# Performance work log

Measured on AMD Instinct MI355X. Metric: run time of the kernel, lower is better.

Reference implementation:

```python
import jax, jax.numpy as jnp
import numpy as np

IGNORE_INDEX = -100
BETA = 0.1

def setup_inputs() -> dict:
    key = jax.random.key(0)
    k1, k2, k3, k4, k5, k6 = jax.random.split(key, 6)
    B, T, H, V = 4, 512, 2048, 32000
    x = jax.random.normal(k1, (B, T, H), dtype=jnp.float32)
    ref_x = jax.random.normal(k2, (B, T, H), dtype=jnp.float32)
    y = jax.random.randint(k3, (B, T), 0, V, dtype=jnp.int64)
    # mask a prefix of each sequence with ignore_index to exercise masking
    y = y.at[:, :10].set(IGNORE_INDEX)
    preference_labels = jax.random.randint(k4, (B,), 0, 2) == 1
    scale = 1.0 / np.sqrt(H)
    W = jax.random.normal(k5, (V, H), dtype=jnp.float32) * scale      # policy lm_head weight
    ref_W = jax.random.normal(k6, (V, H), dtype=jnp.float32) * scale  # reference lm_head weight
    return {"x": x, "ref_x": ref_x, "y": y, "preference_labels": preference_labels,
            "W": W, "ref_W": ref_W}


def _avg_target_logps(inp, w, y):
    # inp: (B, T, H), w: (V, H), y: (B, T) -> per-sequence average log-prob (B,)
    logits = jnp.einsum("bth,vh->btv", inp, w)
    logps = jax.nn.log_softmax(logits.astype(jnp.float32), axis=-1)
    mask = y != IGNORE_INDEX
    labels = jnp.where(mask, y, 0)
    tok_logps = jnp.take_along_axis(logps, labels[..., None], axis=-1)[..., 0]
    return (tok_logps * mask).sum(-1) / mask.sum(-1)


def reference(x, ref_x, y, preference_labels, W, ref_W):
    policy_logps = _avg_target_logps(x, W, y)                              # (B,)
    ref_logps = jax.lax.stop_gradient(_avg_target_logps(ref_x, ref_W, y))  # ref model under no_grad
    logratios = policy_logps - ref_logps
    multiplier = jnp.where(preference_labels, 1.0, -1.0)
    # KTO loss with KL term = 0 (policy_KL_logps / ref_KL_logps are None)
    losses = 1.0 - jax.nn.sigmoid(BETA * logratios * multiplier)
    return losses.sum() / y.shape[0]
```

## Files before the change

### kernel.cpp

```cpp
#include <hip/hip_runtime.h>
#include <math.h>

#define BATCH 4
#define TSEQ 512
#define MTOK 2048
#define HDIM 2048
#define VOCAB 32000
#define NCHUNK 500
#define IGNORE_INDEX (-100)
#define BETA 0.1f

#define CVT_PER_BLOCK 8192
#define WCVT_BLK (VOCAB * HDIM / 4 / CVT_PER_BLOCK)
#define XCVT_BLK (MTOK * HDIM / 4 / CVT_PER_BLOCK)

typedef __attribute__((ext_vector_type(4))) float floatx4;
typedef __attribute__((ext_vector_type(8))) short short8;
typedef __attribute__((ext_vector_type(4))) unsigned short ushortx4;

__device__ __forceinline__ unsigned short f2bf(float f) {
    unsigned int u = __float_as_uint(f);
    u += 0x7fffu + ((u >> 16) & 1u);
    return (unsigned short)(u >> 16);
}

__device__ __forceinline__ void async_copy16(const unsigned short* g, unsigned short* l) {
    __builtin_amdgcn_global_load_lds(
        (const __attribute__((address_space(1))) void*)g,
        (__attribute__((address_space(3))) void*)l, 16, 0, 0);
}

__device__ __forceinline__ void cvt_run(const float* __restrict__ src,
                                        unsigned short* __restrict__ dst,
                                        int relblk) {
    size_t base = (size_t)relblk * CVT_PER_BLOCK + threadIdx.x;
    const floatx4* s4 = (const floatx4*)src;
    ushortx4* d4 = (ushortx4*)dst;
#pragma unroll
    for (int k = 0; k < 32; ++k) {
        floatx4 a = s4[base + k * 256];
        ushortx4 o;
        o[0] = f2bf(a[0]); o[1] = f2bf(a[1]);
        o[2] = f2bf(a[2]); o[3] = f2bf(a[3]);
        d4[base + k * 256] = o;
    }
}

__global__ __launch_bounds__(256) void cvt_all_kernel(
        const float* __restrict__ s0, const float* __restrict__ s1,
        const float* __restrict__ s2, const float* __restrict__ s3,
        unsigned short* __restrict__ d0, unsigned short* __restrict__ d1,
        unsigned short* __restrict__ d2, unsigned short* __restrict__ d3) {
    int b = blockIdx.x;
    if (b < WCVT_BLK)                   cvt_run(s0, d0, b);
    else if (b < 2 * WCVT_BLK)          cvt_run(s1, d1, b - WCVT_BLK);
    else if (b < 2 * WCVT_BLK + XCVT_BLK) cvt_run(s2, d2, b - 2 * WCVT_BLK);
    else                                cvt_run(s3, d3, b - 2 * WCVT_BLK - XCVT_BLK);
}

__global__ __launch_bounds__(256) void cvt_one_kernel(
        const float* __restrict__ src, unsigned short* __restrict__ dst) {
    cvt_run(src, dst, blockIdx.x);
}

#define BK 64
__global__ __launch_bounds__(256, 2) void gemm_lse_kernel(
        const unsigned short* __restrict__ Xb0,
        const unsigned short* __restrict__ Xb1,
        const unsigned short* __restrict__ Wb0,
        const unsigned short* __restrict__ Wb1,
        const int* __restrict__ y,
        float* __restrict__ pmax,
        float* __restrict__ psum,
        float* __restrict__ tlog,
        int slot_base)
{
    __shared__ __align__(16) unsigned short sA[128 * BK];
    __shared__ __align__(16) unsigned short sB[128 * BK];

    const int slot = slot_base + blockIdx.z;
    const unsigned short* __restrict__ Xb = slot ? Xb1 : Xb0;
    const unsigned short* __restrict__ Wb = slot ? Wb1 : Wb0;

    const int tid  = threadIdx.x;
    const int m0   = blockIdx.x * 128;
    const int v0   = blockIdx.y * 128;
    const int w    = tid >> 6;
    const int lane = tid & 63;
    const int wm   = w & 1;
    const int wn   = w >> 1;
    const int c    = lane & 15;
    const int q    = lane >> 4;

    floatx4 acc[4][4] = {};

    const int e0 = tid * 8;

    for (int kt = 0; kt < HDIM / BK; ++kt) {
        const int k0 = kt * BK;
#pragma unroll
        for (int it = 0; it < 4; ++it) {
            int e   = it * 2048 + e0;
            int row = e >> 6;
            int p   = (e >> 3) & 7;
            int col = (p ^ (row & 7)) * 8;
            async_copy16(Xb + (size_t)(m0 + row) * HDIM + (k0 + col), &sA[e]);
            async_copy16(Wb + (size_t)(v0 + row) * HDIM + (k0 + col), &sB[e]);
        }
        __syncthreads();
#pragma unroll
        for (int kk = 0; kk < BK; kk += 32) {
            short8 af[4], bf[4];
            const int gq = (kk >> 3) + q;
            const int pq = gq ^ (c & 7);
#pragma unroll
            for (int i = 0; i < 4; ++i)
                af[i] = *(const short8*)&sA[(wm * 64 + i * 16 + c) * BK + pq * 8];
#pragma unroll
            for (int j = 0; j < 4; ++j)
                bf[j] = *(const short8*)&sB[(wn * 64 + j * 16 + c) * BK + pq * 8];
#pragma unroll
            for (int i = 0; i < 4; ++i)
#pragma unroll
                for (int j = 0; j < 4; ++j)
                    acc[i][j] = __builtin_amdgcn_mfma_f32_16x16x32_bf16(
                        af[i], bf[j], acc[i][j], 0, 0, 0);
        }
        __syncthreads();
    }

    const int chunk = blockIdx.y * 2 + wn;
#pragma unroll
    for (int i = 0; i < 4; ++i) {
        float mx[4], sm[4];
#pragma unroll
        for (int r = 0; r < 4; ++r) {
            float m4 = acc[i][0][r];
            m4 = fmaxf(m4, acc[i][1][r]);
            m4 = fmaxf(m4, acc[i][2][r]);
            m4 = fmaxf(m4, acc[i][3][r]);
            mx[r] = m4;
        }
#pragma unroll
        for (int d = 1; d < 16; d <<= 1)
#pragma unroll
            for (int r = 0; r < 4; ++r)
                mx[r] = fmaxf(mx[r], __shfl_xor(mx[r], d, 64));
#pragma unroll
        for (int r = 0; r < 4; ++r) {
            float s = 0.f;
#pragma unroll
            for (int j = 0; j < 4; ++j) s += expf(acc[i][j][r] - mx[r]);
            sm[r] = s;
        }
#pragma unroll
        for (int d = 1; d < 16; d <<= 1)
#pragma unroll
            for (int r = 0; r < 4; ++r)
                sm[r] += __shfl_xor(sm[r], d, 64);

        const int tokenBase = m0 + wm * 64 + i * 16 + q * 4;
        if (c == 0) {
#pragma unroll
            for (int r = 0; r < 4; ++r) {
                pmax[(size_t)(slot * MTOK + tokenBase + r) * NCHUNK + chunk] = mx[r];
                psum[(size_t)(slot * MTOK + tokenBase + r) * NCHUNK + chunk] = sm[r];
            }
        }
#pragma unroll
        for (int r = 0; r < 4; ++r) {
            int lab = y[tokenBase + r];
            int rel = lab - (v0 + wn * 64);
            if (rel >= 0 && rel < 64 && (rel & 15) == c) {
#pragma unroll
                for (int j = 0; j < 4; ++j)
                    if ((rel >> 4) == j)
                        tlog[(size_t)slot * MTOK + tokenBase + r] = acc[i][j][r];
            }
        }
    }
}

__global__ __launch_bounds__(256) void finalize_kernel(
        const int* __restrict__ y,
        const float* __restrict__ pmax,
        const float* __restrict__ psum,
        const float* __restrict__ tlog,
        float* __restrict__ tokll, int slot_base) {
    const int wv    = threadIdx.x >> 6;
    const int lane  = threadIdx.x & 63;
    const int token = blockIdx.x * 4 + wv;
    const int slot  = slot_base + blockIdx.y;

    const float* pm = &pmax[(size_t)(slot * MTOK + token) * NCHUNK];
    const float* ps = &psum[(size_t)(slot * MTOK + token) * NCHUNK];
    float m = -3.4e38f, s = 0.f;
    for (int c2 = lane; c2 < NCHUNK; c2 += 64) {
        float cm = pm[c2];
        float cs = ps[c2];
        if (cm > m) { s = s * expf(m - cm) + cs; m = cm; }
        else        { s += cs * expf(cm - m); }
    }
#pragma unroll
    for (int d = 1; d < 64; d <<= 1) {
        float om = __shfl_xor(m, d, 64);
        float os = __shfl_xor(s, d, 64);
        if (om > m) { s = s * expf(m - om) + os; m = om; }
        else        { s += os * expf(om - m); }
    }
    if (lane == 0) {
        int lab = y[token];
        float lse = m + logf(s);
        tokll[(size_t)slot * MTOK + token] =
            (lab == IGNORE_INDEX) ? 0.f : (tlog[(size_t)slot * MTOK + token] - lse);
    }
}

__global__ __launch_bounds__(256) void tail_kernel(
        const int* __restrict__ y,
        const float* __restrict__ tokll,
        const int* __restrict__ pref,
        float* __restrict__ out) {
    __shared__ float rs[256];
    __shared__ float rc[256];
    __shared__ float seqavg[8];
    const int tid = threadIdx.x;
    for (int sb = 0; sb < 8; ++sb) {
        const int slot = sb >> 2;
        const int b    = sb & 3;
        float lsum = 0.f, lcnt = 0.f;
        for (int t = tid; t < TSEQ; t += 256) {
            int token = b * TSEQ + t;
            lsum += tokll[(size_t)slot * MTOK + token];
            lcnt += (y[token] != IGNORE_INDEX) ? 1.f : 0.f;
        }
        rs[tid] = lsum; rc[tid] = lcnt;
        __syncthreads();
        for (int s2 = 128; s2 > 0; s2 >>= 1) {
            if (tid < s2) { rs[tid] += rs[tid + s2]; rc[tid] += rc[tid + s2]; }
            __syncthreads();
        }
        if (tid == 0) seqavg[sb] = rs[0] / rc[0];
        __syncthreads();
    }
    if (tid == 0) {
        float acc = 0.f;
        for (int b = 0; b < BATCH; ++b) {
            float lr   = seqavg[b] - seqavg[BATCH + b];
            float mult = pref[b] ? 1.f : -1.f;
            float z    = BETA * lr * mult;
            float sig  = 1.f / (1.f + expf(-z));
            acc += 1.f - sig;
        }
        out[0] = acc * (1.f / (float)BATCH);
    }
}

extern "C" void kernel_launch(void* const* d_in, const int* in_sizes, int n_in,
                              void* d_out, int out_size, void* d_ws, size_t ws_size,
                              hipStream_t stream) {
    const float* x      = (const float*)d_in[0];
    const float* ref_x  = (const float*)d_in[1];
    const int*   y      = (const int*)d_in[2];
    const int*   pref   = (const int*)d_in[3];
    const float* W      = (const float*)d_in[4];
    const float* ref_W  = (const float*)d_in[5];
    float* out = (float*)d_out;
    char*  ws  = (char*)d_ws;

    const size_t WSZ = (size_t)VOCAB * HDIM * 2;
    const size_t XSZ = (size_t)MTOK * HDIM * 2;
    const size_t PSZ = (size_t)2 * MTOK * NCHUNK * 4;

    const size_t need_dual = 2*WSZ + 2*XSZ + 2*PSZ + (size_t)4*MTOK*4 + 4096;

    if (ws_size >= need_dual) {
        unsigned short* wbf0 = (unsigned short*)(ws);
        unsigned short* wbf1 = (unsigned short*)(ws + WSZ);
        unsigned short* xbf0 = (unsigned short*)(ws + 2*WSZ);
        unsigned short* xbf1 = (unsigned short*)(ws + 2*WSZ + XSZ);
        float* pmax  = (float*)(ws + 2*WSZ + 2*XSZ);
        float* psum  = (float*)(ws + 2*WSZ + 2*XSZ + PSZ);
        float* tlog  = (float*)(ws + 2*WSZ + 2*XSZ + 2*PSZ);
        float* tokll = (float*)(ws + 2*WSZ + 2*XSZ + 2*PSZ + (size_t)2*MTOK*4);

        cvt_all_kernel<<<2*WCVT_BLK + 2*XCVT_BLK, 256, 0, stream>>>(
            W, ref_W, x, ref_x, wbf0, wbf1, xbf0, xbf1);
        gemm_lse_kernel<<<dim3(MTOK/128, VOCAB/128, 2), 256, 0, stream>>>(
            xbf0, xbf1, wbf0, wbf1, y, pmax, psum, tlog, 0);
        finalize_kernel<<<dim3(MTOK/4, 2), 256, 0, stream>>>(
            y, pmax, psum, tlog, tokll, 0);
        tail_kernel<<<1, 256, 0, stream>>>(y, tokll, pref, out);
    } else {
        unsigned short* wbf = (unsigned short*)(ws);
        unsigned short* xbf = (unsigned short*)(ws + WSZ);
        float* pmax  = (float*)(ws + WSZ + XSZ);
        float* psum  = (float*)(ws + WSZ + XSZ + PSZ);
        float* tlog  = (float*)(ws + WSZ + XSZ + 2*PSZ);
        float* tokll = (float*)(ws + WSZ + XSZ + 2*PSZ + (size_t)2*MTOK*4);

        for (int model = 0; model < 2; ++model) {
            const float* xin = model ? ref_x : x;
            const float* win = model ? ref_W : W;
            cvt_one_kernel<<<WCVT_BLK, 256, 0, stream>>>(win, wbf);
            cvt_one_kernel<<<XCVT_BLK, 256, 0, stream>>>(xin, xbf);
            gemm_lse_kernel<<<dim3(MTOK/128, VOCAB/128, 1), 256, 0, stream>>>(
                xbf, xbf, wbf, wbf, y, pmax, psum, tlog, model);
            finalize_kernel<<<dim3(MTOK/4, 1), 256, 0, stream>>>(
                y, pmax, psum, tlog, tokll, model);
        }
        tail_kernel<<<1, 256, 0, stream>>>(y, tokll, pref, out);
    }
}
```

Before: 1.111 ms.

## Quantize inputs and weights to FP8 and use scaled FP8 MFMA GEMM

Replaces the bf16 conversion and bf16 MFMA GEMM with FP8 (e4m3) quantization. Weights are pre-scaled by 16 and undone through the scaled MFMA's E8M0 scale operand. The GEMM now uses mfma_scale 16x16x128 f8f6f4 with a 128-wide K tile, which halves operand bytes and uses the higher-throughput FP8 matrix path. The trade is lower precision in the logits feeding log-softmax, which risks accuracy against the fp32 reference.

```diff
diff --git a/kernel.cpp b/kernel.cpp
--- a/kernel.cpp
+++ b/kernel.cpp
@@ -10,77 +10,73 @@
 #define IGNORE_INDEX (-100)
 #define BETA 0.1f
 
+#define WSCALE 16.0f
+#define SCALE_ONE  0x7F7F7F7F
+#define SCALE_W    0x7B7B7B7B
+
 #define CVT_PER_BLOCK 8192
 #define WCVT_BLK (VOCAB * HDIM / 4 / CVT_PER_BLOCK)
 #define XCVT_BLK (MTOK * HDIM / 4 / CVT_PER_BLOCK)
 
 typedef __attribute__((ext_vector_type(4))) float floatx4;
-typedef __attribute__((ext_vector_type(8))) short short8;
-typedef __attribute__((ext_vector_type(4))) unsigned short ushortx4;
-
-__device__ __forceinline__ unsigned short f2bf(float f) {
-    unsigned int u = __float_as_uint(f);
-    u += 0x7fffu + ((u >> 16) & 1u);
-    return (unsigned short)(u >> 16);
-}
-
-__device__ __forceinline__ void async_copy16(const unsigned short* g, unsigned short* l) {
+typedef __attribute__((ext_vector_type(4))) int   intx4;
+typedef __attribute__((ext_vector_type(8))) int   intx8;
+
+__device__ __forceinline__ void async_copy16b(const unsigned char* g, unsigned char* l) {
     __builtin_amdgcn_global_load_lds(
         (const __attribute__((address_space(1))) void*)g,
         (__attribute__((address_space(3))) void*)l, 16, 0, 0);
 }
 
-__device__ __forceinline__ void cvt_run(const float* __restrict__ src,
-                                        unsigned short* __restrict__ dst,
-                                        int relblk) {
+__device__ __forceinline__ void cvtq_run(const float* __restrict__ src,
+                                         unsigned int* __restrict__ dst,
+                                         int relblk, float scale) {
     size_t base = (size_t)relblk * CVT_PER_BLOCK + threadIdx.x;
     const floatx4* s4 = (const floatx4*)src;
-    ushortx4* d4 = (ushortx4*)dst;
 #pragma unroll
     for (int k = 0; k < 32; ++k) {
         floatx4 a = s4[base + k * 256];
-        ushortx4 o;
-        o[0] = f2bf(a[0]); o[1] = f2bf(a[1]);
-        o[2] = f2bf(a[2]); o[3] = f2bf(a[3]);
-        d4[base + k * 256] = o;
-    }
-}
-
-__global__ __launch_bounds__(256) void cvt_all_kernel(
+        int lo  = __builtin_amdgcn_cvt_pk_fp8_f32(a[0] * scale, a[1] * scale, 0,  false);
+        int all = __builtin_amdgcn_cvt_pk_fp8_f32(a[2] * scale, a[3] * scale, lo, true);
+        dst[base + k * 256] = (unsigned int)all;
+    }
+}
+
+__global__ __launch_bounds__(256) void cvtq_all_kernel(
         const float* __restrict__ s0, const float* __restrict__ s1,
         const float* __restrict__ s2, const float* __restrict__ s3,
-        unsigned short* __restrict__ d0, unsigned short* __restrict__ d1,
-        unsigned short* __restrict__ d2, unsigned short* __restrict__ d3) {
+        unsigned int* __restrict__ d0, unsigned int* __restrict__ d1,
+        unsigned int* __restrict__ d2, unsigned int* __restrict__ d3) {
     int b = blockIdx.x;
-    if (b < WCVT_BLK)                   cvt_run(s0, d0, b);
-    else if (b < 2 * WCVT_BLK)          cvt_run(s1, d1, b - WCVT_BLK);
-    else if (b < 2 * WCVT_BLK + XCVT_BLK) cvt_run(s2, d2, b - 2 * WCVT_BLK);
-    else                                cvt_run(s3, d3, b - 2 * WCVT_BLK - XCVT_BLK);
-}
-
-__global__ __launch_bounds__(256) void cvt_one_kernel(
-        const float* __restrict__ src, unsigned short* __restrict__ dst) {
-    cvt_run(src, dst, blockIdx.x);
-}
-
-#define BK 64
-__global__ __launch_bounds__(256, 2) void gemm_lse_kernel(
-        const unsigned short* __restrict__ Xb0,
-        const unsigned short* __restrict__ Xb1,
-        const unsigned short* __restrict__ Wb0,
-        const unsigned short* __restrict__ Wb1,
+    if (b < WCVT_BLK)                     cvtq_run(s0, d0, b, WSCALE);
+    else if (b < 2 * WCVT_BLK)            cvtq_run(s1, d1, b - WCVT_BLK, WSCALE);
+    else if (b < 2 * WCVT_BLK + XCVT_BLK) cvtq_run(s2, d2, b - 2 * WCVT_BLK, 1.0f);
+    else                                  cvtq_run(s3, d3, b - 2 * WCVT_BLK - XCVT_BLK, 1.0f);
+}
+
+__global__ __launch_bounds__(256) void cvtq_one_kernel(
+        const float* __restrict__ src, unsigned int* __restrict__ dst, float scale) {
+    cvtq_run(src, dst, blockIdx.x, scale);
+}
+
+#define BKF 128
+__global__ __launch_bounds__(256, 2) void gemm_lse_fp8_kernel(
+        const unsigned char* __restrict__ Xq0,
+        const unsigned char* __restrict__ Xq1,
+        const unsigned char* __restrict__ Wq0,
+        const unsigned char* __restrict__ Wq1,
         const int* __restrict__ y,
         float* __restrict__ pmax,
         float* __restrict__ psum,
         float* __restrict__ tlog,
         int slot_base)
 {
-    __shared__ __align__(16) unsigned short sA[128 * BK];
-    __shared__ __align__(16) unsigned short sB[128 * BK];
+    __shared__ __align__(16) unsigned char sA[128 * BKF];
+    __shared__ __align__(16) unsigned char sB[128 * BKF];
 
     const int slot = slot_base + blockIdx.z;
-    const unsigned short* __restrict__ Xb = slot ? Xb1 : Xb0;
-    const unsigned short* __restrict__ Wb = slot ? Wb1 : Wb0;
+    const unsigned char* __restrict__ Xq = slot ? Xq1 : Xq0;
+    const unsigned char* __restrict__ Wq = slot ? Wq1 : Wq0;
 
     const int tid  = threadIdx.x;
     const int m0   = blockIdx.x * 128;
@@ -94,38 +90,55 @@
 
     floatx4 acc[4][4] = {};
 
-    const int e0 = tid * 8;
-
-    for (int kt = 0; kt < HDIM / BK; ++kt) {
-        const int k0 = kt * BK;
+    const int e0 = tid * 16;
+
+    for (int kt = 0; kt < HDIM / BKF; ++kt) {
+        const int k0 = kt * BKF;
 #pragma unroll
         for (int it = 0; it < 4; ++it) {
-            int e   = it * 2048 + e0;
-            int row = e >> 6;
-            int p   = (e >> 3) & 7;
-            int col = (p ^ (row & 7)) * 8;
-            async_copy16(Xb + (size_t)(m0 + row) * HDIM + (k0 + col), &sA[e]);
-            async_copy16(Wb + (size_t)(v0 + row) * HDIM + (k0 + col), &sB[e]);
+            int e   = it * 4096 + e0;
+            int row = e >> 7;
+            int p   = (e >> 4) & 7;
+            int col = (p ^ (row & 7)) * 16;
+            async_copy16b(Xq + (size_t)(m0 + row) * HDIM + (k0 + col), &sA[e]);
+            async_copy16b(Wq + (size_t)(v0 + row) * HDIM + (k0 + col), &sB[e]);
         }
         __syncthreads();
-#pragma unroll
-        for (int kk = 0; kk < BK; kk += 32) {
-            short8 af[4], bf[4];
-            const int gq = (kk >> 3) + q;
-            const int pq = gq ^ (c & 7);
-#pragma unroll
-            for (int i = 0; i < 4; ++i)
-                af[i] = *(const short8*)&sA[(wm * 64 + i * 16 + c) * BK + pq * 8];
+
+        intx8 af[4], bf[4];
+#pragma unroll
+        for (int i = 0; i < 4; ++i) {
+            int row = wm * 64 + i * 16 + c;
+            int ch0 = (2 * q)     ^ (row & 7);
+            int ch1 = (2 * q + 1) ^ (row & 7);
+            intx4 lo = *(const intx4*)&sA[row * BKF + ch0 * 16];
+            intx4 hi = *(const intx4*)&sA[row * BKF + ch1 * 16];
+            intx8 v;
+            v[0] = lo[0]; v[1] = lo[1]; v[2] = lo[2]; v[3] = lo[3];
+            v[4] = hi[0]; v[5] = hi[1]; v[6] = hi[2]; v[7] = hi[3];
+            af[i] = v;
+        }
+#pragma unroll
+        for (int j = 0; j < 4; ++j) {
+            int row = wn * 64 + j * 16 + c;
+            int ch0 = (2 * q)     ^ (row & 7);
+            int ch1 = (2 * q + 1) ^ (row & 7);
+            intx4 lo = *(const intx4*)&sB[row * BKF + ch0 * 16];
+            intx4 hi = *(const intx4*)&sB[row * BKF + ch1 * 16];
+            intx8 v;
+            v[0] = lo[0]; v[1] = lo[1]; v[2] = lo[2]; v[3] = lo[3];
+            v[4] = hi[0]; v[5] = hi[1]; v[6] = hi[2]; v[7] = hi[3];
+            bf[j] = v;
+        }
+#pragma unroll
+        for (int i = 0; i < 4; ++i)
 #pragma unroll
             for (int j = 0; j < 4; ++j)
-                bf[j] = *(const short8*)&sB[(wn * 64 + j * 16 + c) * BK + pq * 8];
-#pragma unroll
-            for (int i = 0; i < 4; ++i)
-#pragma unroll
-                for (int j = 0; j < 4; ++j)
-                    acc[i][j] = __builtin_amdgcn_mfma_f32_16x16x32_bf16(
-                        af[i], bf[j], acc[i][j], 0, 0, 0);
-        }
+                acc[i][j] = __builtin_amdgcn_mfma_scale_f32_16x16x128_f8f6f4(
+                    af[i], bf[j], acc[i][j],
+                    0, 0,
+                    0, SCALE_ONE,
+                    0, SCALE_W);
         __syncthreads();
     }
 
@@ -268,44 +281,46 @@
     float* out = (float*)d_out;
     char*  ws  = (char*)d_ws;
 
-    const size_t WSZ = (size_t)VOCAB * HDIM * 2;
-    const size_t XSZ = (size_t)MTOK * HDIM * 2;
-    const size_t PSZ = (size_t)2 * MTOK * NCHUNK * 4;
-
-    const size_t need_dual = 2*WSZ + 2*XSZ + 2*PSZ + (size_t)4*MTOK*4 + 4096;
+    const size_t WQSZ = (size_t)VOCAB * HDIM;
+    const size_t XQSZ = (size_t)MTOK * HDIM;
+    const size_t PSZ  = (size_t)2 * MTOK * NCHUNK * 4;
+
+    const size_t need_dual = 2*WQSZ + 2*XQSZ + 2*PSZ + (size_t)4*MTOK*4 + 4096;
 
     if (ws_size >= need_dual) {
-        unsigned short* wbf0 = (unsigned short*)(ws);
-        unsigned short* wbf1 = (unsigned short*)(ws + WSZ);
-        unsigned short* xbf0 = (unsigned short*)(ws + 2*WSZ);
-        unsigned short* xbf1 = (unsigned short*)(ws + 2*WSZ + XSZ);
-        float* pmax  = (float*)(ws + 2*WSZ + 2*XSZ);
-        float* psum  = (float*)(ws + 2*WSZ + 2*XSZ + PSZ);
-        float* tlog  = (float*)(ws + 2*WSZ + 2*XSZ + 2*PSZ);
-        float* tokll = (float*)(ws + 2*WSZ + 2*XSZ + 2*PSZ + (size_t)2*MTOK*4);
-
-        cvt_all_kernel<<<2*WCVT_BLK + 2*XCVT_BLK, 256, 0, stream>>>(
-            W, ref_W, x, ref_x, wbf0, wbf1, xbf0, xbf1);
-        gemm_lse_kernel<<<dim3(MTOK/128, VOCAB/128, 2), 256, 0, stream>>>(
-            xbf0, xbf1, wbf0, wbf1, y, pmax, psum, tlog, 0);
+        unsigned char* wq0 = (unsigned char*)(ws);
+        unsigned char* wq1 = (unsigned char*)(ws + WQSZ);
+        unsigned char* xq0 = (unsigned char*)(ws + 2*WQSZ);
+        unsigned char* xq1 = (unsigned char*)(ws + 2*WQSZ + XQSZ);
+        float* pmax  = (float*)(ws + 2*WQSZ + 2*XQSZ);
+        float* psum  = (float*)(ws + 2*WQSZ + 2*XQSZ + PSZ);
+        float* tlog  = (float*)(ws + 2*WQSZ + 2*XQSZ + 2*PSZ);
+        float* tokll = (float*)(ws + 2*WQSZ + 2*XQSZ + 2*PSZ + (size_t)2*MTOK*4);
+
+        cvtq_all_kernel<<<2*WCVT_BLK + 2*XCVT_BLK, 256, 0, stream>>>(
+            W, ref_W, x, ref_x,
+            (unsigned int*)wq0, (unsigned int*)wq1,
+            (unsigned int*)xq0, (unsigned int*)xq1);
+        gemm_lse_fp8_kernel<<<dim3(MTOK/128, VOCAB/128, 2), 256, 0, stream>>>(
+            xq0, xq1, wq0, wq1, y, pmax, psum, tlog, 0);
         finalize_kernel<<<dim3(MTOK/4, 2), 256, 0, stream>>>(
             y, pmax, psum, tlog, tokll, 0);
         tail_kernel<<<1, 256, 0, stream>>>(y, tokll, pref, out);
     } else {
-        unsigned short* wbf = (unsigned short*)(ws);
-        unsigned short* xbf = (unsigned short*)(ws + WSZ);
-        float* pmax  = (float*)(ws + WSZ + XSZ);
-        float* psum  = (float*)(ws + WSZ + XSZ + PSZ);
-        float* tlog  = (float*)(ws + WSZ + XSZ + 2*PSZ);
-        float* tokll = (float*)(ws + WSZ + XSZ + 2*PSZ + (size_t)2*MTOK*4);
+        unsigned char* wq = (unsigned char*)(ws);
+        unsigned char* xq = (unsigned char*)(ws + WQSZ);
+        float* pmax  = (float*)(ws + WQSZ + XQSZ);
+        float* psum  = (float*)(ws + WQSZ + XQSZ + PSZ);
+        float* tlog  = (float*)(ws + WQSZ + XQSZ + 2*PSZ);
+        float* tokll = (float*)(ws + WQSZ + XQSZ + 2*PSZ + (size_t)2*MTOK*4);
 
         for (int model = 0; model < 2; ++model) {
             const float* xin = model ? ref_x : x;
             const float* win = model ? ref_W : W;
-            cvt_one_kernel<<<WCVT_BLK, 256, 0, stream>>>(win, wbf);
-            cvt_one_kernel<<<XCVT_BLK, 256, 0, stream>>>(xin, xbf);
-            gemm_lse_kernel<<<dim3(MTOK/128, VOCAB/128, 1), 256, 0, stream>>>(
-                xbf, xbf, wbf, wbf, y, pmax, psum, tlog, model);
+            cvtq_one_kernel<<<WCVT_BLK, 256, 0, stream>>>(win, (unsigned int*)wq, WSCALE);
+            cvtq_one_kernel<<<XCVT_BLK, 256, 0, stream>>>(xin, (unsigned int*)xq, 1.0f);
+            gemm_lse_fp8_kernel<<<dim3(MTOK/128, VOCAB/128, 1), 256, 0, stream>>>(
+                xq, xq, wq, wq, y, pmax, psum, tlog, model);
             finalize_kernel<<<dim3(MTOK/4, 1), 256, 0, stream>>>(
                 y, pmax, psum, tlog, tokll, model);
         }
```

Result: faster. 1.013 ms (-8.8%).
